# Kernel optimization log

Hardware: AMD Instinct MI355X
Metric: run time of the kernel (lower is better)

The kernel has to match this reference:

```python
import jax, jax.numpy as jnp
import numpy as np

N = 65536      # total nodes = B * MAXN
E = 524288     # edges (avg degree 8)
DX = 32; DG = 32
IN_DIM = DX + 3 * DG   # 128, after concat(x, g0, g1, g2)
H = 256; OUT = 8; MAXN = 8192


def setup_inputs() -> dict:
    key = jax.random.key(0)
    ks = jax.random.split(key, 40)
    inp = {}
    inp['x'] = jax.random.normal(ks[0], (N, DX), jnp.float32)
    inp['g0'] = jax.random.normal(ks[1], (N, DG), jnp.float32)
    inp['g1'] = jax.random.normal(ks[2], (N, DG), jnp.float32)
    inp['g2'] = jax.random.normal(ks[3], (N, DG), jnp.float32)
    inp['edge_src'] = jax.random.randint(ks[4], (E,), 0, N, jnp.int32)
    inp['edge_dst'] = jax.random.randint(ks[5], (E,), 0, N, jnp.int32)
    dims = [(IN_DIM, H), (H, H), (H, H), (H, H)]
    k = 6
    for i, (di, do) in enumerate(dims):
        s = 1.0 / np.sqrt(di)
        inp[f'Wl{i}'] = jax.random.uniform(ks[k], (di, do), jnp.float32, -s, s); k += 1
        inp[f'Wr{i}'] = jax.random.uniform(ks[k], (di, do), jnp.float32, -s, s); k += 1
        inp[f'b{i}'] = jnp.zeros((do,), jnp.float32)
    s = 1.0 / np.sqrt(MAXN)
    inp['mlp1_W1'] = jax.random.uniform(ks[k], (MAXN, H), jnp.float32, -s, s); k += 1
    inp['mlp1_b1'] = jnp.zeros((H,), jnp.float32)
    s = 1.0 / np.sqrt(H)
    inp['mlp1_W2'] = jax.random.uniform(ks[k], (H, 1), jnp.float32, -s, s); k += 1
    inp['mlp1_b2'] = jnp.zeros((1,), jnp.float32)
    inp['bn_gamma'] = jnp.ones((H,), jnp.float32)
    inp['bn_beta'] = jnp.zeros((H,), jnp.float32)
    inp['mlp2_W1'] = jax.random.uniform(ks[k], (H, H), jnp.float32, -s, s); k += 1
    inp['mlp2_b1'] = jnp.zeros((H,), jnp.float32)
    inp['mlp2_W2'] = jax.random.uniform(ks[k], (H, OUT), jnp.float32, -s, s); k += 1
    inp['mlp2_b2'] = jnp.zeros((OUT,), jnp.float32)
    return inp


def _forward(x, g0, g1, g2, edge_src, edge_dst,
             Wl0, Wr0, b0, Wl1, Wr1, b1, Wl2, Wr2, b2, Wl3, Wr3, b3,
             mlp1_W1, mlp1_b1, mlp1_W2, mlp1_b2, bn_gamma, bn_beta,
             mlp2_W1, mlp2_b1, mlp2_W2, mlp2_b2):
    h = jnp.concatenate([x, g0, g1, g2], axis=1)  # [N, IN_DIM]
    # mean-aggregation denominator (in-degree, clamped at 1 like PyG mean)
    cnt = jnp.maximum(
        jax.ops.segment_sum(jnp.ones((E,), h.dtype), edge_dst, num_segments=N), 1.0)
    for Wl, Wr, b in ((Wl0, Wr0, b0), (Wl1, Wr1, b1), (Wl2, Wr2, b2), (Wl3, Wr3, b3)):
        agg = jax.ops.segment_sum(h[edge_src], edge_dst, num_segments=N) / cnt[:, None]
        # SAGEConv: lin_l(mean of neighbors) + lin_r(self) + bias, then ReLU
        h = jax.nn.relu(agg @ Wl + h @ Wr + b)
        # F.dropout in eval / deterministic reference: identity
    h = h.reshape(-1, H, MAXN)                               # [B, H, MAXN]
    h = jax.nn.relu(jnp.einsum('bhm,mk->bhk', h, mlp1_W1) + mlp1_b1)
    h = (jnp.einsum('bhk,ko->bho', h, mlp1_W2) + mlp1_b2)[..., 0]  # [B, H]
    mean = h.mean(axis=0)
    var = h.var(axis=0)
    h = (h - mean) / jnp.sqrt(var + 1e-5) * bn_gamma + bn_beta
    h = jax.nn.relu(h)
    h = jax.nn.relu(h @ mlp2_W1 + mlp2_b1)
    return h @ mlp2_W2 + mlp2_b2                              # [B, OUT]


def reference(x, g0, g1, g2, edge_src, edge_dst,
              Wl0, Wr0, b0, Wl1, Wr1, b1, Wl2, Wr2, b2, Wl3, Wr3, b3,
              mlp1_W1, mlp1_b1, mlp1_W2, mlp1_b2, bn_gamma, bn_beta,
              mlp2_W1, mlp2_b1, mlp2_W2, mlp2_b2):
    return _forward(x, g0, g1, g2, edge_src, edge_dst,
                    Wl0, Wr0, b0, Wl1, Wr1, b1, Wl2, Wr2, b2, Wl3, Wr3, b3,
                    mlp1_W1, mlp1_b1, mlp1_W2, mlp1_b2, bn_gamma, bn_beta,
                    mlp2_W1, mlp2_b1, mlp2_W2, mlp2_b2)
```

## Files before the change

### kernel.cpp

```cpp
#include <hip/hip_runtime.h>
#include <hip/hip_bf16.h>


#define NN 65536
#define EE 524288
#define ROWS 65537
#define PCSR_CAP 720896

using frag16 = __attribute__((ext_vector_type(8))) short;
using f32x4  = __attribute__((ext_vector_type(4))) float;

__device__ __forceinline__ float b2f(unsigned short u) {
    union { unsigned u32; float f; } x; x.u32 = (unsigned)u << 16; return x.f;
}

__device__ __forceinline__ void gld_lds16(const void* g, void* l) {
    __builtin_amdgcn_global_load_lds(
        (const __attribute__((address_space(1))) void*)g,
        (__attribute__((address_space(3))) void*)l, 16, 0, 0);
}


__global__ void gs_zero_deg(int* deg) {
    int i = blockIdx.x * 256 + threadIdx.x;
    if (i < NN) deg[i] = 0;
}

__global__ void gs_hist(const int* __restrict__ dst, int* __restrict__ deg) {
    int e = blockIdx.x * 256 + threadIdx.x;
    atomicAdd(&deg[dst[e]], 1);
}

__global__ void gs_deg_reduce(const int* __restrict__ deg, int* __restrict__ bsum) {
    int t = threadIdx.x;
    int p = (deg[blockIdx.x * 256 + t] + 3) & ~3;
#pragma unroll
    for (int off = 32; off > 0; off >>= 1) p += __shfl_down(p, off);
    __shared__ int w4[4];
    if ((t & 63) == 0) w4[t >> 6] = p;
    __syncthreads();
    if (t == 0) bsum[blockIdx.x] = w4[0] + w4[1] + w4[2] + w4[3];
}

__global__ void gs_scan_bsum(const int* __restrict__ bsum, int* __restrict__ bofs,
                             int* __restrict__ prow) {
    __shared__ int part[256];
    int t = threadIdx.x;
    int v = bsum[t];
    part[t] = v;
    __syncthreads();
    for (int off = 1; off < 256; off <<= 1) {
        int add = (t >= off) ? part[t - off] : 0;
        __syncthreads();
        part[t] += add;
        __syncthreads();
    }
    bofs[t] = part[t] - v;
    if (t == 255) prow[NN] = part[255];
}

__global__ void gs_scan_apply(const int* __restrict__ deg, const int* __restrict__ bofs,
                              int* __restrict__ prow, int* __restrict__ cursor,
                              float* __restrict__ inv_cnt, int* __restrict__ pcsr,
                              __hip_bfloat16* __restrict__ P0,
                              __hip_bfloat16* __restrict__ P1) {
    __shared__ int part[256];
    int t = threadIdx.x;
    int i = blockIdx.x * 256 + t;
    int d = deg[i];
    int p = (d + 3) & ~3;
    part[t] = p;
    __syncthreads();
    for (int off = 1; off < 256; off <<= 1) {
        int add = (t >= off) ? part[t - off] : 0;
        __syncthreads();
        part[t] += add;
        __syncthreads();
    }
    int beg = bofs[blockIdx.x] + part[t] - p;
    prow[i] = beg;
    cursor[i] = beg;
    inv_cnt[i] = 1.0f / (float)(d > 0 ? d : 1);
    for (int j = d; j < p; ++j) pcsr[beg + j] = NN;
    if (blockIdx.x == 0) {
        ((unsigned*)(P0 + (size_t)NN * 512))[t] = 0u;
        ((unsigned*)(P1 + (size_t)NN * 512))[t] = 0u;
    }
}

__global__ void gs_bucket(const int* __restrict__ src, const int* __restrict__ dst,
                          int* __restrict__ cursor, int* __restrict__ pcsr) {
    int e = blockIdx.x * 256 + threadIdx.x;
    int d = dst[e];
    int p = atomicAdd(&cursor[d], 1);
    pcsr[p] = src[e];
}

struct TcvtArgs {
    const float* src[8];
    __hip_bfloat16* dst[8];
    int ldk[8];
    int kofs[8];
    int kblk[8];
};

__global__ void gs_tcvt_all(TcvtArgs a) {
    int z = blockIdx.z;
    if ((int)blockIdx.x >= a.kblk[z]) return;
    const float* src = a.src[z];
    __hip_bfloat16* dst = a.dst[z];
    int ldk = a.ldk[z], kofs = a.kofs[z];
    __shared__ float tile[32][33];
    int kb = blockIdx.x * 32, nb = blockIdx.y * 32;
    int tx = threadIdx.x, ty = threadIdx.y;
#pragma unroll
    for (int i = 0; i < 32; i += 8)
        tile[ty + i][tx] = src[(size_t)(kb + ty + i) * 256 + nb + tx];
    __syncthreads();
#pragma unroll
    for (int i = 0; i < 32; i += 8) {
        int n = nb + ty + i, k = kb + tx;
        dst[(size_t)n * ldk + kofs + k] = __float2bfloat16(tile[tx][ty + i]);
    }
}

__global__ void gs_tcvt(const float* __restrict__ src, __hip_bfloat16* __restrict__ dst,
                        int ldk, int kofs) {
    __shared__ float tile[32][33];
    int kb = blockIdx.x * 32, nb = blockIdx.y * 32;
    int tx = threadIdx.x, ty = threadIdx.y;
#pragma unroll
    for (int i = 0; i < 32; i += 8)
        tile[ty + i][tx] = src[(size_t)(kb + ty + i) * 256 + nb + tx];
    __syncthreads();
#pragma unroll
    for (int i = 0; i < 32; i += 8) {
        int n = nb + ty + i, k = kb + tx;
        dst[(size_t)n * ldk + kofs + k] = __float2bfloat16(tile[tx][ty + i]);
    }
}

__global__ void gs_concat_bf(const float* __restrict__ x, const float* __restrict__ g0,
                             const float* __restrict__ g1, const float* __restrict__ g2,
                             __hip_bfloat16* __restrict__ h) {
    int idx = blockIdx.x * 256 + threadIdx.x;
    int n = idx >> 7, c = idx & 127;
    float v;
    if (c < 32)       v = x[n * 32 + c];
    else if (c < 64)  v = g0[n * 32 + (c - 32)];
    else if (c < 96)  v = g1[n * 32 + (c - 64)];
    else              v = g2[n * 32 + (c - 96)];
    h[(size_t)n * 512 + 256 + c] = __float2bfloat16(v);
}

template <int DIM>
__global__ void gs_agg_bf(const __hip_bfloat16* __restrict__ hsrc,
                          __hip_bfloat16* __restrict__ adst,
                          const int* __restrict__ prow, const int* __restrict__ pcsr,
                          const float* __restrict__ inv_cnt) {
    int wave = threadIdx.x >> 6;
    int lane = threadIdx.x & 63;
    int n = blockIdx.x * 4 + wave;
    int e = prow[n], pe = prow[n + 1];
    float iv = inv_cnt[n];
    if constexpr (DIM == 256) {
        const __hip_bfloat16* base = hsrc + lane * 4;
        float a0 = 0.f, a1 = 0.f, a2 = 0.f, a3 = 0.f;
        int4 s4;
        if (e < pe) s4 = *(const int4*)(pcsr + e);
        while (e < pe) {
            int4 cur = s4;
            e += 4;
            if (e < pe) s4 = *(const int4*)(pcsr + e);
            ushort4 v0 = *(const ushort4*)(base + (size_t)cur.x * 512);
            ushort4 v1 = *(const ushort4*)(base + (size_t)cur.y * 512);
            ushort4 v2 = *(const ushort4*)(base + (size_t)cur.z * 512);
            ushort4 v3 = *(const ushort4*)(base + (size_t)cur.w * 512);
            a0 += b2f(v0.x); a1 += b2f(v0.y); a2 += b2f(v0.z); a3 += b2f(v0.w);
            a0 += b2f(v1.x); a1 += b2f(v1.y); a2 += b2f(v1.z); a3 += b2f(v1.w);
            a0 += b2f(v2.x); a1 += b2f(v2.y); a2 += b2f(v2.z); a3 += b2f(v2.w);
            a0 += b2f(v3.x); a1 += b2f(v3.y); a2 += b2f(v3.z); a3 += b2f(v3.w);
        }
        __hip_bfloat16 o[4] = {__float2bfloat16(a0 * iv), __float2bfloat16(a1 * iv),
                               __float2bfloat16(a2 * iv), __float2bfloat16(a3 * iv)};
        *(ushort4*)(adst + (size_t)n * 512 + lane * 4) = *(const ushort4*)o;
    } else {
        const __hip_bfloat16* base = hsrc + lane * 2;
        float a0 = 0.f, a1 = 0.f;
        int4 s4;
        if (e < pe) s4 = *(const int4*)(pcsr + e);
        while (e < pe) {
            int4 cur = s4;
            e += 4;
            if (e < pe) s4 = *(const int4*)(pcsr + e);
            ushort2 v0 = *(const ushort2*)(base + (size_t)cur.x * 512);
            ushort2 v1 = *(const ushort2*)(base + (size_t)cur.y * 512);
            ushort2 v2 = *(const ushort2*)(base + (size_t)cur.z * 512);
            ushort2 v3 = *(const ushort2*)(base + (size_t)cur.w * 512);
            a0 += b2f(v0.x); a1 += b2f(v0.y);
            a0 += b2f(v1.x); a1 += b2f(v1.y);
            a0 += b2f(v2.x); a1 += b2f(v2.y);
            a0 += b2f(v3.x); a1 += b2f(v3.y);
        }
        __hip_bfloat16 o[2] = {__float2bfloat16(a0 * iv), __float2bfloat16(a1 * iv)};
        *(ushort2*)(adst + (size_t)n * 512 + lane * 2) = *(const ushort2*)o;
    }
}

__device__ __forceinline__ void mfma_block(const __hip_bfloat16* A, int lda,
                                           const __hip_bfloat16* Bt, int ldb,
                                           int kbeg, int kend, size_t row0, size_t nbase,
                                           __hip_bfloat16* As, __hip_bfloat16* Bs,
                                           f32x4 acc[4][4]) {
    const int t = threadIdx.x;
    const int lane = t & 63;
    const int w = t >> 6;
    const int wr = (w >> 1) * 64;
    const int wc = (w & 1) * 64;
    const int srow = w * 32 + (lane >> 3);
    const int scol = (lane & 7) * 8;
    for (int kc = kbeg; kc < kend; kc += 64) {
#pragma unroll
        for (int l = 0; l < 4; ++l) {
            gld_lds16(A + (row0 + srow + 8 * l) * (size_t)lda + kc + scol,
                      As + (w * 32 + 8 * l) * 64);
            gld_lds16(Bt + (nbase + srow + 8 * l) * (size_t)ldb + kc + scol,
                      Bs + (w * 32 + 8 * l) * 64);
        }
        __syncthreads();
#pragma unroll
        for (int kk = 0; kk < 64; kk += 32) {
            frag16 af[4], bf[4];
#pragma unroll
            for (int i = 0; i < 4; ++i)
                af[i] = *(const frag16*)(As + (wr + i * 16 + (lane & 15)) * 64 + kk + (lane >> 4) * 8);
#pragma unroll
            for (int j = 0; j < 4; ++j)
                bf[j] = *(const frag16*)(Bs + (wc + j * 16 + (lane & 15)) * 64 + kk + (lane >> 4) * 8);
#pragma unroll
            for (int i = 0; i < 4; ++i)
#pragma unroll
                for (int j = 0; j < 4; ++j)
                    acc[i][j] = __builtin_amdgcn_mfma_f32_16x16x32_bf16(af[i], bf[j], acc[i][j], 0, 0, 0);
        }
        __syncthreads();
    }
}

__global__ __launch_bounds__(256, 2)
void gs_gemm_bias_relu(const __hip_bfloat16* __restrict__ A, int lda, int K,
                       const __hip_bfloat16* __restrict__ Bt, int ldb,
                       const float* __restrict__ bias,
                       __hip_bfloat16* __restrict__ C, int ldc, int cofs) {
    __shared__ __hip_bfloat16 As[128 * 64];
    __shared__ __hip_bfloat16 Bs[128 * 64];
    f32x4 acc[4][4] = {};
    const size_t row0 = (size_t)blockIdx.x * 128;
    const size_t nbase = (size_t)blockIdx.y * 128;
    mfma_block(A, lda, Bt, ldb, 0, K, row0, nbase, As, Bs, acc);
    const int lane = threadIdx.x & 63;
    const int w = threadIdx.x >> 6;
    const int wr = (w >> 1) * 64, wc = (w & 1) * 64;
#pragma unroll
    for (int j = 0; j < 4; ++j) {
        int n = (int)nbase + wc + j * 16 + (lane & 15);
        float bv = bias[n];
#pragma unroll
        for (int i = 0; i < 4; ++i) {
#pragma unroll
            for (int r = 0; r < 4; ++r) {
                size_t row = row0 + wr + i * 16 + (lane >> 4) * 4 + r;
                C[row * (size_t)ldc + cofs + n] = __float2bfloat16(fmaxf(acc[i][j][r] + bv, 0.f));
            }
        }
    }
}

__global__ __launch_bounds__(256, 2)
void gs_gemm_splitk(const __hip_bfloat16* __restrict__ A, int lda,
                    const __hip_bfloat16* __restrict__ Bt, int ldb,
                    float* __restrict__ part) {
    __shared__ __hip_bfloat16 As[128 * 64];
    __shared__ __hip_bfloat16 Bs[128 * 64];
    f32x4 acc[4][4] = {};
    const size_t row0 = (size_t)blockIdx.x * 128;
    const size_t nbase = (size_t)blockIdx.y * 128;
    const int kbeg = blockIdx.z * 512;
    mfma_block(A, lda, Bt, ldb, kbeg, kbeg + 512, row0, nbase, As, Bs, acc);
    const int lane = threadIdx.x & 63;
    const int w = threadIdx.x >> 6;
    const int wr = (w >> 1) * 64, wc = (w & 1) * 64;
    float* p = part + (size_t)blockIdx.z * 2048 * 256;
#pragma unroll
    for (int j = 0; j < 4; ++j) {
        int n = (int)nbase + wc + j * 16 + (lane & 15);
#pragma unroll
        for (int i = 0; i < 4; ++i) {
#pragma unroll
            for (int r = 0; r < 4; ++r) {
                size_t row = row0 + wr + i * 16 + (lane >> 4) * 4 + r;
                p[row * 256 + n] = acc[i][j][r];
            }
        }
    }
}

__global__ void gs_mlp1_reduce(const float* __restrict__ part, const float* __restrict__ b1,
                               float* __restrict__ t1) {
    int idx = blockIdx.x * 256 + threadIdx.x;
    float s = 0.f;
#pragma unroll
    for (int ks = 0; ks < 16; ++ks) s += part[(size_t)ks * 524288 + idx];
    s += b1[idx & 255];
    t1[idx] = fmaxf(s, 0.f);
}

__global__ void gs_pool(const float* __restrict__ t1, const float* __restrict__ W2,
                        const float* __restrict__ b2, float* __restrict__ pooled) {
    int r = blockIdx.x;
    int l = threadIdx.x;
    float acc = 0.f;
#pragma unroll
    for (int q = 0; q < 4; ++q) {
        int c = l + q * 64;
        acc = fmaf(t1[(size_t)r * 256 + c], W2[c], acc);
    }
    for (int off = 32; off > 0; off >>= 1) acc += __shfl_down(acc, off);
    if (l == 0) pooled[r] = acc + b2[0];
}

__global__ void gs_bn_mlp2(const float* __restrict__ pooled, const float* __restrict__ gamma,
                           const float* __restrict__ beta, const float* __restrict__ W1,
                           const float* __restrict__ b1, const float* __restrict__ W2,
                           const float* __restrict__ b2, float* __restrict__ out) {
    __shared__ float hb[8][256];
    __shared__ float h2[8][256];
    int t = threadIdx.x;
    {
        float v[8];
        float m = 0.f;
#pragma unroll
        for (int b = 0; b < 8; ++b) { v[b] = pooled[b * 256 + t]; m += v[b]; }
        m *= 0.125f;
        float var = 0.f;
#pragma unroll
        for (int b = 0; b < 8; ++b) { float d = v[b] - m; var += d * d; }
        var *= 0.125f;
        float is = 1.0f / sqrtf(var + 1e-5f);
        float g = gamma[t], bt = beta[t];
#pragma unroll
        for (int b = 0; b < 8; ++b) hb[b][t] = fmaxf((v[b] - m) * is * g + bt, 0.f);
    }
    __syncthreads();
    {
        float acc[8] = {};
        for (int i = 0; i < 256; ++i) {
            float w = W1[i * 256 + t];
#pragma unroll
            for (int b = 0; b < 8; ++b) acc[b] = fmaf(hb[b][i], w, acc[b]);
        }
        float bb = b1[t];
#pragma unroll
        for (int b = 0; b < 8; ++b) h2[b][t] = fmaxf(acc[b] + bb, 0.f);
    }
    __syncthreads();
    if (t < 64) {
        int b = t >> 3, o = t & 7;
        float acc = 0.f;
        for (int j = 0; j < 256; ++j) acc = fmaf(h2[b][j], W2[j * 8 + o], acc);
        out[b * 8 + o] = acc + b2[o];
    }
}

extern "C" void kernel_launch(void* const* d_in, const int* in_sizes, int n_in,
                              void* d_out, int out_size, void* d_ws, size_t ws_size,
                              hipStream_t stream) {
    const float* x  = (const float*)d_in[0];
    const float* g0 = (const float*)d_in[1];
    const float* g1 = (const float*)d_in[2];
    const float* g2 = (const float*)d_in[3];
    const int* edge_src = (const int*)d_in[4];
    const int* edge_dst = (const int*)d_in[5];
    const float* Wl[4] = {(const float*)d_in[6], (const float*)d_in[9],
                          (const float*)d_in[12], (const float*)d_in[15]};
    const float* Wr[4] = {(const float*)d_in[7], (const float*)d_in[10],
                          (const float*)d_in[13], (const float*)d_in[16]};
    const float* bs[4] = {(const float*)d_in[8], (const float*)d_in[11],
                          (const float*)d_in[14], (const float*)d_in[17]};
    const float* mlp1_W1 = (const float*)d_in[18];
    const float* mlp1_b1 = (const float*)d_in[19];
    const float* mlp1_W2 = (const float*)d_in[20];
    const float* mlp1_b2 = (const float*)d_in[21];
    const float* bn_gamma = (const float*)d_in[22];
    const float* bn_beta  = (const float*)d_in[23];
    const float* mlp2_W1 = (const float*)d_in[24];
    const float* mlp2_b1 = (const float*)d_in[25];
    const float* mlp2_W2 = (const float*)d_in[26];
    const float* mlp2_b2 = (const float*)d_in[27];
    float* out = (float*)d_out;

    char* ws = (char*)d_ws;
    __hip_bfloat16* P0 = (__hip_bfloat16*)ws;
    __hip_bfloat16* P1 = P0 + (size_t)ROWS * 512;
    __hip_bfloat16* WC0 = P1 + (size_t)ROWS * 512;
    __hip_bfloat16* WC1 = WC0 + 65536;
    __hip_bfloat16* WC2 = WC1 + 131072;
    __hip_bfloat16* WC3 = WC2 + 131072;
    __hip_bfloat16* W1T = WC3 + 131072;
    float* inv_cnt = (float*)(W1T + 2097152);
    int* ideg = (int*)(inv_cnt + 65536);
    int* prow = ideg + 65536;
    int* cursor = prow + 65544;
    int* bsum = cursor + 65536;
    int* bofs = bsum + 256;
    int* pcsr = bofs + 256;
    __hip_bfloat16* H4 = P0;
    float* T1 = (float*)P1;
    float* pooled = T1 + 524288;
    float* PART = (float*)((char*)P1 + (size_t)(4 << 20));

    gs_zero_deg<<<256, 256, 0, stream>>>(ideg);
    gs_hist<<<EE / 256, 256, 0, stream>>>(edge_dst, ideg);
    gs_deg_reduce<<<256, 256, 0, stream>>>(ideg, bsum);
    gs_scan_bsum<<<1, 256, 0, stream>>>(bsum, bofs, prow);
    gs_scan_apply<<<256, 256, 0, stream>>>(ideg, bofs, prow, cursor, inv_cnt, pcsr, P0, P1);
    gs_bucket<<<EE / 256, 256, 0, stream>>>(edge_src, edge_dst, cursor, pcsr);

    {
        TcvtArgs a;
        const float* srcs[8] = {Wl[0], Wr[0], Wl[1], Wr[1], Wl[2], Wr[2], Wl[3], Wr[3]};
        __hip_bfloat16* dsts[8] = {WC0, WC0, WC1, WC1, WC2, WC2, WC3, WC3};
        int ldks[8] = {256, 256, 512, 512, 512, 512, 512, 512};
        int kofss[8] = {0, 128, 0, 256, 0, 256, 0, 256};
        int kblks[8] = {4, 4, 8, 8, 8, 8, 8, 8};
        for (int i = 0; i < 8; ++i) {
            a.src[i] = srcs[i]; a.dst[i] = dsts[i];
            a.ldk[i] = ldks[i]; a.kofs[i] = kofss[i]; a.kblk[i] = kblks[i];
        }
        gs_tcvt_all<<<dim3(8, 8, 8), dim3(32, 8), 0, stream>>>(a);
    }
    gs_tcvt<<<dim3(256, 8), dim3(32, 8), 0, stream>>>(mlp1_W1, W1T, 8192, 0);

    gs_concat_bf<<<NN * 128 / 256, 256, 0, stream>>>(x, g0, g1, g2, P0);

    gs_agg_bf<128><<<NN / 4, 256, 0, stream>>>(P0 + 256, P0 + 128, prow, pcsr, inv_cnt);
    gs_gemm_bias_relu<<<dim3(NN / 128, 2), 256, 0, stream>>>(P0 + 128, 512, 256, WC0, 256,
                                                             bs[0], P1, 512, 256);
    gs_agg_bf<256><<<NN / 4, 256, 0, stream>>>(P1 + 256, P1, prow, pcsr, inv_cnt);
    gs_gemm_bias_relu<<<dim3(NN / 128, 2), 256, 0, stream>>>(P1, 512, 512, WC1, 512,
                                                             bs[1], P0, 512, 256);
    gs_agg_bf<256><<<NN / 4, 256, 0, stream>>>(P0 + 256, P0, prow, pcsr, inv_cnt);
    gs_gemm_bias_relu<<<dim3(NN / 128, 2), 256, 0, stream>>>(P0, 512, 512, WC2, 512,
                                                             bs[2], P1, 512, 256);
    gs_agg_bf<256><<<NN / 4, 256, 0, stream>>>(P1 + 256, P1, prow, pcsr, inv_cnt);
    gs_gemm_bias_relu<<<dim3(NN / 128, 2), 256, 0, stream>>>(P1, 512, 512, WC3, 512,
                                                             bs[3], H4, 256, 0);

    gs_gemm_splitk<<<dim3(16, 2, 16), 256, 0, stream>>>(H4, 8192, W1T, 8192, PART);
    gs_mlp1_reduce<<<2048, 256, 0, stream>>>(PART, mlp1_b1, T1);
    gs_pool<<<2048, 64, 0, stream>>>(T1, mlp1_W2, mlp1_b2, pooled);

    gs_bn_mlp2<<<1, 256, 0, stream>>>(pooled, bn_gamma, bn_beta, mlp2_W1, mlp2_b1,
                                      mlp2_W2, mlp2_b2, out);
}
```

Measured before the change: 516.0 us.

## Unroll neighbor gather by 8, transpose MFMA outputs for vector stores, halve split-K

The aggregation loop now loads eight neighbor indices per iteration, without the software prefetch, so more gathers are in flight at once. The last group of four is padded with index NN, which assumes row NN of the source buffer holds zeros. The MFMA operand order is swapped so each lane holds four consecutive output columns. This lets the GEMM epilogues write packed ushort4 bf16 and float4 partials instead of scalar strided stores. The mlp1 split-K drops from 16 to 8 slices, which halves the partial traffic and the reduce work but leaves fewer blocks to run in parallel.

```diff
diff --git a/kernel.cpp b/kernel.cpp
--- a/kernel.cpp
+++ b/kernel.cpp
@@ -12,6 +12,10 @@
 
 __device__ __forceinline__ float b2f(unsigned short u) {
     union { unsigned u32; float f; } x; x.u32 = (unsigned)u << 16; return x.f;
+}
+
+__device__ __forceinline__ unsigned short f2b(float f) {
+    return (unsigned short)(__bfloat16_as_ushort(__float2bfloat16(f)));
 }
 
 __device__ __forceinline__ void gld_lds16(const void* g, void* l) {
@@ -166,20 +170,28 @@
     if constexpr (DIM == 256) {
         const __hip_bfloat16* base = hsrc + lane * 4;
         float a0 = 0.f, a1 = 0.f, a2 = 0.f, a3 = 0.f;
-        int4 s4;
-        if (e < pe) s4 = *(const int4*)(pcsr + e);
         while (e < pe) {
-            int4 cur = s4;
-            e += 4;
-            if (e < pe) s4 = *(const int4*)(pcsr + e);
-            ushort4 v0 = *(const ushort4*)(base + (size_t)cur.x * 512);
-            ushort4 v1 = *(const ushort4*)(base + (size_t)cur.y * 512);
-            ushort4 v2 = *(const ushort4*)(base + (size_t)cur.z * 512);
-            ushort4 v3 = *(const ushort4*)(base + (size_t)cur.w * 512);
+            int4 ia = *(const int4*)(pcsr + e);
+            int4 ib;
+            if (e + 4 < pe) ib = *(const int4*)(pcsr + e + 4);
+            else            ib = make_int4(NN, NN, NN, NN);
+            e += 8;
+            ushort4 v0 = *(const ushort4*)(base + (size_t)ia.x * 512);
+            ushort4 v1 = *(const ushort4*)(base + (size_t)ia.y * 512);
+            ushort4 v2 = *(const ushort4*)(base + (size_t)ia.z * 512);
+            ushort4 v3 = *(const ushort4*)(base + (size_t)ia.w * 512);
+            ushort4 v4 = *(const ushort4*)(base + (size_t)ib.x * 512);
+            ushort4 v5 = *(const ushort4*)(base + (size_t)ib.y * 512);
+            ushort4 v6 = *(const ushort4*)(base + (size_t)ib.z * 512);
+            ushort4 v7 = *(const ushort4*)(base + (size_t)ib.w * 512);
             a0 += b2f(v0.x); a1 += b2f(v0.y); a2 += b2f(v0.z); a3 += b2f(v0.w);
             a0 += b2f(v1.x); a1 += b2f(v1.y); a2 += b2f(v1.z); a3 += b2f(v1.w);
             a0 += b2f(v2.x); a1 += b2f(v2.y); a2 += b2f(v2.z); a3 += b2f(v2.w);
             a0 += b2f(v3.x); a1 += b2f(v3.y); a2 += b2f(v3.z); a3 += b2f(v3.w);
+            a0 += b2f(v4.x); a1 += b2f(v4.y); a2 += b2f(v4.z); a3 += b2f(v4.w);
+            a0 += b2f(v5.x); a1 += b2f(v5.y); a2 += b2f(v5.z); a3 += b2f(v5.w);
+            a0 += b2f(v6.x); a1 += b2f(v6.y); a2 += b2f(v6.z); a3 += b2f(v6.w);
+            a0 += b2f(v7.x); a1 += b2f(v7.y); a2 += b2f(v7.z); a3 += b2f(v7.w);
         }
         __hip_bfloat16 o[4] = {__float2bfloat16(a0 * iv), __float2bfloat16(a1 * iv),
                                __float2bfloat16(a2 * iv), __float2bfloat16(a3 * iv)};
@@ -187,20 +199,28 @@
     } else {
         const __hip_bfloat16* base = hsrc + lane * 2;
         float a0 = 0.f, a1 = 0.f;
-        int4 s4;
-        if (e < pe) s4 = *(const int4*)(pcsr + e);
         while (e < pe) {
-            int4 cur = s4;
-            e += 4;
-            if (e < pe) s4 = *(const int4*)(pcsr + e);
-            ushort2 v0 = *(const ushort2*)(base + (size_t)cur.x * 512);
-            ushort2 v1 = *(const ushort2*)(base + (size_t)cur.y * 512);
-            ushort2 v2 = *(const ushort2*)(base + (size_t)cur.z * 512);
-            ushort2 v3 = *(const ushort2*)(base + (size_t)cur.w * 512);
+            int4 ia = *(const int4*)(pcsr + e);
+            int4 ib;
+            if (e + 4 < pe) ib = *(const int4*)(pcsr + e + 4);
+            else            ib = make_int4(NN, NN, NN, NN);
+            e += 8;
+            ushort2 v0 = *(const ushort2*)(base + (size_t)ia.x * 512);
+            ushort2 v1 = *(const ushort2*)(base + (size_t)ia.y * 512);
+            ushort2 v2 = *(const ushort2*)(base + (size_t)ia.z * 512);
+            ushort2 v3 = *(const ushort2*)(base + (size_t)ia.w * 512);
+            ushort2 v4 = *(const ushort2*)(base + (size_t)ib.x * 512);
+            ushort2 v5 = *(const ushort2*)(base + (size_t)ib.y * 512);
+            ushort2 v6 = *(const ushort2*)(base + (size_t)ib.z * 512);
+            ushort2 v7 = *(const ushort2*)(base + (size_t)ib.w * 512);
             a0 += b2f(v0.x); a1 += b2f(v0.y);
             a0 += b2f(v1.x); a1 += b2f(v1.y);
             a0 += b2f(v2.x); a1 += b2f(v2.y);
             a0 += b2f(v3.x); a1 += b2f(v3.y);
+            a0 += b2f(v4.x); a1 += b2f(v4.y);
+            a0 += b2f(v5.x); a1 += b2f(v5.y);
+            a0 += b2f(v6.x); a1 += b2f(v6.y);
+            a0 += b2f(v7.x); a1 += b2f(v7.y);
         }
         __hip_bfloat16 o[2] = {__float2bfloat16(a0 * iv), __float2bfloat16(a1 * iv)};
         *(ushort2*)(adst + (size_t)n * 512 + lane * 2) = *(const ushort2*)o;
@@ -241,7 +261,7 @@
             for (int i = 0; i < 4; ++i)
 #pragma unroll
                 for (int j = 0; j < 4; ++j)
-                    acc[i][j] = __builtin_amdgcn_mfma_f32_16x16x32_bf16(af[i], bf[j], acc[i][j], 0, 0, 0);
+                    acc[i][j] = __builtin_amdgcn_mfma_f32_16x16x32_bf16(bf[j], af[i], acc[i][j], 0, 0, 0);
         }
         __syncthreads();
     }
@@ -263,15 +283,17 @@
     const int wr = (w >> 1) * 64, wc = (w & 1) * 64;
 #pragma unroll
     for (int j = 0; j < 4; ++j) {
-        int n = (int)nbase + wc + j * 16 + (lane & 15);
-        float bv = bias[n];
+        int nb = wc + j * 16 + (lane >> 4) * 4;
+        const float4 bv = *(const float4*)&bias[(int)nbase + nb];
 #pragma unroll
         for (int i = 0; i < 4; ++i) {
-#pragma unroll
-            for (int r = 0; r < 4; ++r) {
-                size_t row = row0 + wr + i * 16 + (lane >> 4) * 4 + r;
-                C[row * (size_t)ldc + cofs + n] = __float2bfloat16(fmaxf(acc[i][j][r] + bv, 0.f));
-            }
+            int m = wr + i * 16 + (lane & 15);
+            unsigned short o[4];
+            o[0] = f2b(fmaxf(acc[i][j][0] + bv.x, 0.f));
+            o[1] = f2b(fmaxf(acc[i][j][1] + bv.y, 0.f));
+            o[2] = f2b(fmaxf(acc[i][j][2] + bv.z, 0.f));
+            o[3] = f2b(fmaxf(acc[i][j][3] + bv.w, 0.f));
+            *(ushort4*)(C + (row0 + m) * (size_t)ldc + cofs + nbase + nb) = *(const ushort4*)o;
         }
     }
 }
@@ -285,22 +307,19 @@
     f32x4 acc[4][4] = {};
     const size_t row0 = (size_t)blockIdx.x * 128;
     const size_t nbase = (size_t)blockIdx.y * 128;
-    const int kbeg = blockIdx.z * 512;
-    mfma_block(A, lda, Bt, ldb, kbeg, kbeg + 512, row0, nbase, As, Bs, acc);
+    const int kbeg = blockIdx.z * 1024;
+    mfma_block(A, lda, Bt, ldb, kbeg, kbeg + 1024, row0, nbase, As, Bs, acc);
     const int lane = threadIdx.x & 63;
     const int w = threadIdx.x >> 6;
     const int wr = (w >> 1) * 64, wc = (w & 1) * 64;
     float* p = part + (size_t)blockIdx.z * 2048 * 256;
 #pragma unroll
     for (int j = 0; j < 4; ++j) {
-        int n = (int)nbase + wc + j * 16 + (lane & 15);
+        int nb = wc + j * 16 + (lane >> 4) * 4;
 #pragma unroll
         for (int i = 0; i < 4; ++i) {
-#pragma unroll
-            for (int r = 0; r < 4; ++r) {
-                size_t row = row0 + wr + i * 16 + (lane >> 4) * 4 + r;
-                p[row * 256 + n] = acc[i][j][r];
-            }
+            int m = wr + i * 16 + (lane & 15);
+            *(f32x4*)(p + (row0 + m) * 256 + nbase + nb) = acc[i][j];
         }
     }
 }
@@ -310,7 +329,7 @@
     int idx = blockIdx.x * 256 + threadIdx.x;
     float s = 0.f;
 #pragma unroll
-    for (int ks = 0; ks < 16; ++ks) s += part[(size_t)ks * 524288 + idx];
+    for (int ks = 0; ks < 8; ++ks) s += part[(size_t)ks * 524288 + idx];
     s += b1[idx & 255];
     t1[idx] = fmaxf(s, 0.f);
 }
@@ -456,7 +475,7 @@
     gs_gemm_bias_relu<<<dim3(NN / 128, 2), 256, 0, stream>>>(P1, 512, 512, WC3, 512,
                                                              bs[3], H4, 256, 0);
 
-    gs_gemm_splitk<<<dim3(16, 2, 16), 256, 0, stream>>>(H4, 8192, W1T, 8192, PART);
+    gs_gemm_splitk<<<dim3(16, 2, 8), 256, 0, stream>>>(H4, 8192, W1T, 8192, PART);
     gs_mlp1_reduce<<<2048, 256, 0, stream>>>(PART, mlp1_b1, T1);
     gs_pool<<<2048, 64, 0, stream>>>(T1, mlp1_W2, mlp1_b2, pooled);
 
```

After: 531.8 us. 3.1% more time.

## Degree-sort aggregation nodes, vectorize GEMM epilogue stores, halve split-K count

Applied to the files above, without the earlier changes.

Builds a degree histogram and a permutation that orders nodes by descending in-degree, so each aggregation block processes waves with similar edge counts. It also swaps the MFMA operand order so each lane holds four consecutive output columns, which lets the GEMM epilogues issue ushort4/float4 stores instead of scalar ones. The split-K GEMM drops from 16 to 8 K-slices, which shrinks the partial buffer and the reduction work. The degree ordering gives up the locality of sequential node order in the aggregation writes, and replaces the zeroing kernel with a memset.

```diff
diff --git a/kernel.cpp b/kernel.cpp
--- a/kernel.cpp
+++ b/kernel.cpp
@@ -14,6 +14,10 @@
     union { unsigned u32; float f; } x; x.u32 = (unsigned)u << 16; return x.f;
 }
 
+__device__ __forceinline__ unsigned short f2b(float f) {
+    return (unsigned short)(__bfloat16_as_ushort(__float2bfloat16(f)));
+}
+
 __device__ __forceinline__ void gld_lds16(const void* g, void* l) {
     __builtin_amdgcn_global_load_lds(
         (const __attribute__((address_space(1))) void*)g,
@@ -21,29 +25,32 @@
 }
 
 
-__global__ void gs_zero_deg(int* deg) {
-    int i = blockIdx.x * 256 + threadIdx.x;
-    if (i < NN) deg[i] = 0;
-}
-
 __global__ void gs_hist(const int* __restrict__ dst, int* __restrict__ deg) {
     int e = blockIdx.x * 256 + threadIdx.x;
     atomicAdd(&deg[dst[e]], 1);
 }
 
-__global__ void gs_deg_reduce(const int* __restrict__ deg, int* __restrict__ bsum) {
+__global__ void gs_deg_reduce(const int* __restrict__ deg, int* __restrict__ bsum,
+                              int* __restrict__ dhist) {
+    __shared__ int lh[64];
     int t = threadIdx.x;
-    int p = (deg[blockIdx.x * 256 + t] + 3) & ~3;
+    if (t < 64) lh[t] = 0;
+    __syncthreads();
+    int d = deg[blockIdx.x * 256 + t];
+    atomicAdd(&lh[min(d, 63)], 1);
+    int p = (d + 3) & ~3;
 #pragma unroll
     for (int off = 32; off > 0; off >>= 1) p += __shfl_down(p, off);
     __shared__ int w4[4];
     if ((t & 63) == 0) w4[t >> 6] = p;
     __syncthreads();
     if (t == 0) bsum[blockIdx.x] = w4[0] + w4[1] + w4[2] + w4[3];
+    if (t < 64 && lh[t]) atomicAdd(&dhist[t], lh[t]);
 }
 
 __global__ void gs_scan_bsum(const int* __restrict__ bsum, int* __restrict__ bofs,
-                             int* __restrict__ prow) {
+                             int* __restrict__ prow, const int* __restrict__ dhist,
+                             int* __restrict__ dcur) {
     __shared__ int part[256];
     int t = threadIdx.x;
     int v = bsum[t];
@@ -57,11 +64,16 @@
     }
     bofs[t] = part[t] - v;
     if (t == 255) prow[NN] = part[255];
+    if (t == 0) {
+        int run = 0;
+        for (int b = 63; b >= 0; --b) { dcur[b] = run; run += dhist[b]; }
+    }
 }
 
 __global__ void gs_scan_apply(const int* __restrict__ deg, const int* __restrict__ bofs,
                               int* __restrict__ prow, int* __restrict__ cursor,
                               float* __restrict__ inv_cnt, int* __restrict__ pcsr,
+                              int* __restrict__ dcur, int* __restrict__ perm,
                               __hip_bfloat16* __restrict__ P0,
                               __hip_bfloat16* __restrict__ P1) {
     __shared__ int part[256];
@@ -82,6 +94,8 @@
     cursor[i] = beg;
     inv_cnt[i] = 1.0f / (float)(d > 0 ? d : 1);
     for (int j = d; j < p; ++j) pcsr[beg + j] = NN;
+    int pos = atomicAdd(&dcur[min(d, 63)], 1);
+    perm[pos] = i;
     if (blockIdx.x == 0) {
         ((unsigned*)(P0 + (size_t)NN * 512))[t] = 0u;
         ((unsigned*)(P1 + (size_t)NN * 512))[t] = 0u;
@@ -157,10 +171,11 @@
 __global__ void gs_agg_bf(const __hip_bfloat16* __restrict__ hsrc,
                           __hip_bfloat16* __restrict__ adst,
                           const int* __restrict__ prow, const int* __restrict__ pcsr,
-                          const float* __restrict__ inv_cnt) {
+                          const float* __restrict__ inv_cnt,
+                          const int* __restrict__ perm) {
     int wave = threadIdx.x >> 6;
     int lane = threadIdx.x & 63;
-    int n = blockIdx.x * 4 + wave;
+    int n = perm[blockIdx.x * 4 + wave];
     int e = prow[n], pe = prow[n + 1];
     float iv = inv_cnt[n];
     if constexpr (DIM == 256) {
@@ -241,7 +256,7 @@
             for (int i = 0; i < 4; ++i)
 #pragma unroll
                 for (int j = 0; j < 4; ++j)
-                    acc[i][j] = __builtin_amdgcn_mfma_f32_16x16x32_bf16(af[i], bf[j], acc[i][j], 0, 0, 0);
+                    acc[i][j] = __builtin_amdgcn_mfma_f32_16x16x32_bf16(bf[j], af[i], acc[i][j], 0, 0, 0);
         }
         __syncthreads();
     }
@@ -263,15 +278,17 @@
     const int wr = (w >> 1) * 64, wc = (w & 1) * 64;
 #pragma unroll
     for (int j = 0; j < 4; ++j) {
-        int n = (int)nbase + wc + j * 16 + (lane & 15);
-        float bv = bias[n];
+        int nb = wc + j * 16 + (lane >> 4) * 4;
+        const float4 bv = *(const float4*)&bias[(int)nbase + nb];
 #pragma unroll
         for (int i = 0; i < 4; ++i) {
-#pragma unroll
-            for (int r = 0; r < 4; ++r) {
-                size_t row = row0 + wr + i * 16 + (lane >> 4) * 4 + r;
-                C[row * (size_t)ldc + cofs + n] = __float2bfloat16(fmaxf(acc[i][j][r] + bv, 0.f));
-            }
+            int m = wr + i * 16 + (lane & 15);
+            unsigned short o[4];
+            o[0] = f2b(fmaxf(acc[i][j][0] + bv.x, 0.f));
+            o[1] = f2b(fmaxf(acc[i][j][1] + bv.y, 0.f));
+            o[2] = f2b(fmaxf(acc[i][j][2] + bv.z, 0.f));
+            o[3] = f2b(fmaxf(acc[i][j][3] + bv.w, 0.f));
+            *(ushort4*)(C + (row0 + m) * (size_t)ldc + cofs + nbase + nb) = *(const ushort4*)o;
         }
     }
 }
@@ -285,22 +302,19 @@
     f32x4 acc[4][4] = {};
     const size_t row0 = (size_t)blockIdx.x * 128;
     const size_t nbase = (size_t)blockIdx.y * 128;
-    const int kbeg = blockIdx.z * 512;
-    mfma_block(A, lda, Bt, ldb, kbeg, kbeg + 512, row0, nbase, As, Bs, acc);
+    const int kbeg = blockIdx.z * 1024;
+    mfma_block(A, lda, Bt, ldb, kbeg, kbeg + 1024, row0, nbase, As, Bs, acc);
     const int lane = threadIdx.x & 63;
     const int w = threadIdx.x >> 6;
     const int wr = (w >> 1) * 64, wc = (w & 1) * 64;
     float* p = part + (size_t)blockIdx.z * 2048 * 256;
 #pragma unroll
     for (int j = 0; j < 4; ++j) {
-        int n = (int)nbase + wc + j * 16 + (lane & 15);
+        int nb = wc + j * 16 + (lane >> 4) * 4;
 #pragma unroll
         for (int i = 0; i < 4; ++i) {
-#pragma unroll
-            for (int r = 0; r < 4; ++r) {
-                size_t row = row0 + wr + i * 16 + (lane >> 4) * 4 + r;
-                p[row * 256 + n] = acc[i][j][r];
-            }
+            int m = wr + i * 16 + (lane & 15);
+            *(f32x4*)(p + (row0 + m) * 256 + nbase + nb) = acc[i][j];
         }
     }
 }
@@ -310,7 +324,7 @@
     int idx = blockIdx.x * 256 + threadIdx.x;
     float s = 0.f;
 #pragma unroll
-    for (int ks = 0; ks < 16; ++ks) s += part[(size_t)ks * 524288 + idx];
+    for (int ks = 0; ks < 8; ++ks) s += part[(size_t)ks * 524288 + idx];
     s += b1[idx & 255];
     t1[idx] = fmaxf(s, 0.f);
 }
@@ -409,21 +423,25 @@
     __hip_bfloat16* W1T = WC3 + 131072;
     float* inv_cnt = (float*)(W1T + 2097152);
     int* ideg = (int*)(inv_cnt + 65536);
-    int* prow = ideg + 65536;
+    int* dhist = ideg + 65536;
+    int* dcur = dhist + 64;
+    int* prow = dcur + 64;
     int* cursor = prow + 65544;
     int* bsum = cursor + 65536;
     int* bofs = bsum + 256;
-    int* pcsr = bofs + 256;
+    int* perm = bofs + 256;
+    int* pcsr = perm + 65536;
     __hip_bfloat16* H4 = P0;
     float* T1 = (float*)P1;
     float* pooled = T1 + 524288;
     float* PART = (float*)((char*)P1 + (size_t)(4 << 20));
 
-    gs_zero_deg<<<256, 256, 0, stream>>>(ideg);
+    hipMemsetAsync(ideg, 0, (65536 + 64) * sizeof(int), stream);
     gs_hist<<<EE / 256, 256, 0, stream>>>(edge_dst, ideg);
-    gs_deg_reduce<<<256, 256, 0, stream>>>(ideg, bsum);
-    gs_scan_bsum<<<1, 256, 0, stream>>>(bsum, bofs, prow);
-    gs_scan_apply<<<256, 256, 0, stream>>>(ideg, bofs, prow, cursor, inv_cnt, pcsr, P0, P1);
+    gs_deg_reduce<<<256, 256, 0, stream>>>(ideg, bsum, dhist);
+    gs_scan_bsum<<<1, 256, 0, stream>>>(bsum, bofs, prow, dhist, dcur);
+    gs_scan_apply<<<256, 256, 0, stream>>>(ideg, bofs, prow, cursor, inv_cnt, pcsr,
+                                           dcur, perm, P0, P1);
     gs_bucket<<<EE / 256, 256, 0, stream>>>(edge_src, edge_dst, cursor, pcsr);
 
     {
@@ -443,20 +461,20 @@
 
     gs_concat_bf<<<NN * 128 / 256, 256, 0, stream>>>(x, g0, g1, g2, P0);
 
-    gs_agg_bf<128><<<NN / 4, 256, 0, stream>>>(P0 + 256, P0 + 128, prow, pcsr, inv_cnt);
+    gs_agg_bf<128><<<NN / 4, 256, 0, stream>>>(P0 + 256, P0 + 128, prow, pcsr, inv_cnt, perm);
     gs_gemm_bias_relu<<<dim3(NN / 128, 2), 256, 0, stream>>>(P0 + 128, 512, 256, WC0, 256,
                                                              bs[0], P1, 512, 256);
-    gs_agg_bf<256><<<NN / 4, 256, 0, stream>>>(P1 + 256, P1, prow, pcsr, inv_cnt);
+    gs_agg_bf<256><<<NN / 4, 256, 0, stream>>>(P1 + 256, P1, prow, pcsr, inv_cnt, perm);
     gs_gemm_bias_relu<<<dim3(NN / 128, 2), 256, 0, stream>>>(P1, 512, 512, WC1, 512,
                                                              bs[1], P0, 512, 256);
-    gs_agg_bf<256><<<NN / 4, 256, 0, stream>>>(P0 + 256, P0, prow, pcsr, inv_cnt);
+    gs_agg_bf<256><<<NN / 4, 256, 0, stream>>>(P0 + 256, P0, prow, pcsr, inv_cnt, perm);
     gs_gemm_bias_relu<<<dim3(NN / 128, 2), 256, 0, stream>>>(P0, 512, 512, WC2, 512,
                                                              bs[2], P1, 512, 256);
-    gs_agg_bf<256><<<NN / 4, 256, 0, stream>>>(P1 + 256, P1, prow, pcsr, inv_cnt);
+    gs_agg_bf<256><<<NN / 4, 256, 0, stream>>>(P1 + 256, P1, prow, pcsr, inv_cnt, perm);
     gs_gemm_bias_relu<<<dim3(NN / 128, 2), 256, 0, stream>>>(P1, 512, 512, WC3, 512,
                                                              bs[3], H4, 256, 0);
 
-    gs_gemm_splitk<<<dim3(16, 2, 16), 256, 0, stream>>>(H4, 8192, W1T, 8192, PART);
+    gs_gemm_splitk<<<dim3(16, 2, 8), 256, 0, stream>>>(H4, 8192, W1T, 8192, PART);
     gs_mlp1_reduce<<<2048, 256, 0, stream>>>(PART, mlp1_b1, T1);
     gs_pool<<<2048, 64, 0, stream>>>(T1, mlp1_W2, mlp1_b2, pooled);
 
```

Measured after the change: 772.0 us. 1.5x slower.

## Vectorize GEMM epilogue stores, pad CSR for unconditional prefetch, halve split-K

Applied to the files above, without the earlier changes.

Swaps the MFMA operand order so each lane holds four consecutive output columns. The GEMM epilogues can then write packed ushort4 bf16 or float4 partials, with a vector bias load, instead of scattered scalar stores. The aggregation kernels drop the bounds check on the index prefetch, and the CSR buffer is padded with sentinel entries so the over-read stays safe. The mlp1 split-K factor goes from 16 to 8, which halves the partial-sum traffic and the reduce work but gives fewer blocks to fill the GPU.

```diff
diff --git a/kernel.cpp b/kernel.cpp
--- a/kernel.cpp
+++ b/kernel.cpp
@@ -5,13 +5,17 @@
 #define NN 65536
 #define EE 524288
 #define ROWS 65537
-#define PCSR_CAP 720896
+#define PCSR_CAP 720904
 
 using frag16 = __attribute__((ext_vector_type(8))) short;
 using f32x4  = __attribute__((ext_vector_type(4))) float;
 
 __device__ __forceinline__ float b2f(unsigned short u) {
     union { unsigned u32; float f; } x; x.u32 = (unsigned)u << 16; return x.f;
+}
+
+__device__ __forceinline__ unsigned short f2b(float f) {
+    return (unsigned short)(__bfloat16_as_ushort(__float2bfloat16(f)));
 }
 
 __device__ __forceinline__ void gld_lds16(const void* g, void* l) {
@@ -85,6 +89,7 @@
     if (blockIdx.x == 0) {
         ((unsigned*)(P0 + (size_t)NN * 512))[t] = 0u;
         ((unsigned*)(P1 + (size_t)NN * 512))[t] = 0u;
+        if (t < 8) pcsr[PCSR_CAP - 8 + t] = NN;
     }
 }
 
@@ -166,12 +171,11 @@
     if constexpr (DIM == 256) {
         const __hip_bfloat16* base = hsrc + lane * 4;
         float a0 = 0.f, a1 = 0.f, a2 = 0.f, a3 = 0.f;
-        int4 s4;
-        if (e < pe) s4 = *(const int4*)(pcsr + e);
+        int4 s4 = *(const int4*)(pcsr + e);
         while (e < pe) {
             int4 cur = s4;
             e += 4;
-            if (e < pe) s4 = *(const int4*)(pcsr + e);
+            s4 = *(const int4*)(pcsr + e);
             ushort4 v0 = *(const ushort4*)(base + (size_t)cur.x * 512);
             ushort4 v1 = *(const ushort4*)(base + (size_t)cur.y * 512);
             ushort4 v2 = *(const ushort4*)(base + (size_t)cur.z * 512);
@@ -187,12 +191,11 @@
     } else {
         const __hip_bfloat16* base = hsrc + lane * 2;
         float a0 = 0.f, a1 = 0.f;
-        int4 s4;
-        if (e < pe) s4 = *(const int4*)(pcsr + e);
+        int4 s4 = *(const int4*)(pcsr + e);
         while (e < pe) {
             int4 cur = s4;
             e += 4;
-            if (e < pe) s4 = *(const int4*)(pcsr + e);
+            s4 = *(const int4*)(pcsr + e);
             ushort2 v0 = *(const ushort2*)(base + (size_t)cur.x * 512);
             ushort2 v1 = *(const ushort2*)(base + (size_t)cur.y * 512);
             ushort2 v2 = *(const ushort2*)(base + (size_t)cur.z * 512);
@@ -241,7 +244,7 @@
             for (int i = 0; i < 4; ++i)
 #pragma unroll
                 for (int j = 0; j < 4; ++j)
-                    acc[i][j] = __builtin_amdgcn_mfma_f32_16x16x32_bf16(af[i], bf[j], acc[i][j], 0, 0, 0);
+                    acc[i][j] = __builtin_amdgcn_mfma_f32_16x16x32_bf16(bf[j], af[i], acc[i][j], 0, 0, 0);
         }
         __syncthreads();
     }
@@ -263,15 +266,17 @@
     const int wr = (w >> 1) * 64, wc = (w & 1) * 64;
 #pragma unroll
     for (int j = 0; j < 4; ++j) {
-        int n = (int)nbase + wc + j * 16 + (lane & 15);
-        float bv = bias[n];
+        int nb = wc + j * 16 + (lane >> 4) * 4;
+        const float4 bv = *(const float4*)&bias[(int)nbase + nb];
 #pragma unroll
         for (int i = 0; i < 4; ++i) {
-#pragma unroll
-            for (int r = 0; r < 4; ++r) {
-                size_t row = row0 + wr + i * 16 + (lane >> 4) * 4 + r;
-                C[row * (size_t)ldc + cofs + n] = __float2bfloat16(fmaxf(acc[i][j][r] + bv, 0.f));
-            }
+            int m = wr + i * 16 + (lane & 15);
+            unsigned short o[4];
+            o[0] = f2b(fmaxf(acc[i][j][0] + bv.x, 0.f));
+            o[1] = f2b(fmaxf(acc[i][j][1] + bv.y, 0.f));
+            o[2] = f2b(fmaxf(acc[i][j][2] + bv.z, 0.f));
+            o[3] = f2b(fmaxf(acc[i][j][3] + bv.w, 0.f));
+            *(ushort4*)(C + (row0 + m) * (size_t)ldc + cofs + nbase + nb) = *(const ushort4*)o;
         }
     }
 }
@@ -285,22 +290,19 @@
     f32x4 acc[4][4] = {};
     const size_t row0 = (size_t)blockIdx.x * 128;
     const size_t nbase = (size_t)blockIdx.y * 128;
-    const int kbeg = blockIdx.z * 512;
-    mfma_block(A, lda, Bt, ldb, kbeg, kbeg + 512, row0, nbase, As, Bs, acc);
+    const int kbeg = blockIdx.z * 1024;
+    mfma_block(A, lda, Bt, ldb, kbeg, kbeg + 1024, row0, nbase, As, Bs, acc);
     const int lane = threadIdx.x & 63;
     const int w = threadIdx.x >> 6;
     const int wr = (w >> 1) * 64, wc = (w & 1) * 64;
     float* p = part + (size_t)blockIdx.z * 2048 * 256;
 #pragma unroll
     for (int j = 0; j < 4; ++j) {
-        int n = (int)nbase + wc + j * 16 + (lane & 15);
+        int nb = wc + j * 16 + (lane >> 4) * 4;
 #pragma unroll
         for (int i = 0; i < 4; ++i) {
-#pragma unroll
-            for (int r = 0; r < 4; ++r) {
-                size_t row = row0 + wr + i * 16 + (lane >> 4) * 4 + r;
-                p[row * 256 + n] = acc[i][j][r];
-            }
+            int m = wr + i * 16 + (lane & 15);
+            *(f32x4*)(p + (row0 + m) * 256 + nbase + nb) = acc[i][j];
         }
     }
 }
@@ -310,7 +312,7 @@
     int idx = blockIdx.x * 256 + threadIdx.x;
     float s = 0.f;
 #pragma unroll
-    for (int ks = 0; ks < 16; ++ks) s += part[(size_t)ks * 524288 + idx];
+    for (int ks = 0; ks < 8; ++ks) s += part[(size_t)ks * 524288 + idx];
     s += b1[idx & 255];
     t1[idx] = fmaxf(s, 0.f);
 }
@@ -456,7 +458,7 @@
     gs_gemm_bias_relu<<<dim3(NN / 128, 2), 256, 0, stream>>>(P1, 512, 512, WC3, 512,
                                                              bs[3], H4, 256, 0);
 
-    gs_gemm_splitk<<<dim3(16, 2, 16), 256, 0, stream>>>(H4, 8192, W1T, 8192, PART);
+    gs_gemm_splitk<<<dim3(16, 2, 8), 256, 0, stream>>>(H4, 8192, W1T, 8192, PART);
     gs_mlp1_reduce<<<2048, 256, 0, stream>>>(PART, mlp1_b1, T1);
     gs_pool<<<2048, 64, 0, stream>>>(T1, mlp1_W2, mlp1_b2, pooled);
 
```

New measurement: 542.8 us. 1.05x slower.
